# Kernel tuning notes

Measured on AMD Instinct MI355X. Metric: run time of the kernel, lower is better.

## Reference

```python
import jax, jax.numpy as jnp
import numpy as np

N_NODES = 100000
N_EDGES = 800000
# (in_dim, out_channels_per_head, heads) for the 5 stacked GATConv layers
DIMS = [(32, 24, 10), (240, 24, 5), (120, 24, 2), (48, 24, 1), (24, 12, 1)]
NEG_SLOPE = 0.2  # PyG GATConv default leaky_relu slope


def setup_inputs() -> dict:
    key = jax.random.key(0)
    ks = jax.random.split(key, 4 + 4 * len(DIMS))
    x = jax.random.normal(ks[0], (N_NODES, 32), jnp.float32)
    # edge_index with no self loops (dst = src + nonzero offset mod N),
    # since PyG GATConv removes then re-adds self loops.
    src = jax.random.randint(ks[1], (N_EDGES,), 0, N_NODES)
    off = jax.random.randint(ks[2], (N_EDGES,), 1, N_NODES)
    dst = (src + off) % N_NODES
    edge_index = jnp.stack([src, dst]).astype(jnp.int32)
    edge_attr = jax.random.normal(ks[3], (N_EDGES, 4), jnp.float32)
    inp = {"x": x, "edge_index": edge_index, "edge_attr": edge_attr}
    for i, (din, c, h) in enumerate(DIMS):
        kw, kb, ka, kd = ks[4 + 4 * i: 8 + 4 * i]
        s = 1.0 / np.sqrt(din)
        inp[f"W{i}"] = jax.random.normal(kw, (din, h * c), jnp.float32) * s
        inp[f"b{i}"] = jax.random.normal(kb, (h * c,), jnp.float32) * 0.01
        inp[f"as{i}"] = jax.random.normal(ka, (h, c), jnp.float32) * (1.0 / np.sqrt(c))
        inp[f"ad{i}"] = jax.random.normal(kd, (h, c), jnp.float32) * (1.0 / np.sqrt(c))
    return inp


def gat_layer(x, src, dst, W, b, a_src, a_dst):
    # Faithful PyG GATConv (concat=True, bias=True, edge_dim=None)
    n = x.shape[0]
    h_heads, c = a_src.shape
    h = (x @ W).reshape(n, h_heads, c)                      # [N,H,C]
    alpha_s = jnp.einsum('nhc,hc->nh', h, a_src)            # [N,H]
    alpha_d = jnp.einsum('nhc,hc->nh', h, a_dst)            # [N,H]
    e = jax.nn.leaky_relu(alpha_s[src] + alpha_d[dst], NEG_SLOPE)  # [E,H]
    # segment softmax over incoming edges of each destination node
    m = jax.ops.segment_max(e, dst, num_segments=n)         # [N,H]
    ex = jnp.exp(e - m[dst])
    z = jax.ops.segment_sum(ex, dst, num_segments=n)        # [N,H]
    attn = ex / z[dst]                                      # [E,H]
    out = jax.ops.segment_sum(h[src] * attn[:, :, None], dst, num_segments=n)
    return out.reshape(n, h_heads * c) + b


def reference(x, edge_index, edge_attr,
              W0, b0, as0, ad0, W1, b1, as1, ad1, W2, b2, as2, ad2,
              W3, b3, as3, ad3, W4, b4, as4, ad4):
    # edge_attr is ignored: GATConv(edge_dim=None) does not use it.
    n = x.shape[0]
    loop = jnp.arange(n, dtype=edge_index.dtype)
    src = jnp.concatenate([edge_index[0], loop])  # add self loops (PyG default)
    dst = jnp.concatenate([edge_index[1], loop])
    params = [(W0, b0, as0, ad0), (W1, b1, as1, ad1), (W2, b2, as2, ad2),
              (W3, b3, as3, ad3), (W4, b4, as4, ad4)]
    for W, b, a_s, a_d in params:
        x = jax.nn.relu(gat_layer(x, src, dst, W, b, a_s, a_d))
    return x
```

## Files before the change

kernel.cpp:

```cpp
#include <hip/hip_runtime.h>
#include <math.h>

#define NN 100000
#define EE 800000
#define ET (EE + NN)
#define BS 256
#define BKTS 391
#define FB_EPB 4096
#define LDSCAP 4096
#define DBINS 64

typedef _Float16 f16;
typedef __attribute__((ext_vector_type(4))) _Float16 half4;
typedef __attribute__((ext_vector_type(8))) _Float16 half8;
typedef __attribute__((ext_vector_type(4))) float f32x4;
template<int V> struct HV;
template<> struct HV<4>{ typedef half4 type; };
template<> struct HV<8>{ typedef half8 type; };

static inline int cdiv(long a, int b){ return (int)((a + b - 1) / b); }

__global__ __launch_bounds__(256) void k_bhist(const int* __restrict__ ei,
                                               int* __restrict__ bucketCount){
    __shared__ int hist[BKTS];
    for (int t = threadIdx.x; t < BKTS; t += 256) hist[t] = 0;
    __syncthreads();
    const int e0 = blockIdx.x * FB_EPB + threadIdx.x;
    #pragma unroll
    for (int i = 0; i < 16; i++){
        int e = e0 + i * 256;
        if (e < ET){
            int d = (e < EE) ? ei[EE + e] : (e - EE);
            atomicAdd(&hist[d >> 8], 1);
        }
    }
    __syncthreads();
    for (int t = threadIdx.x; t < BKTS; t += 256){
        int c = hist[t];
        if (c) atomicAdd(&bucketCount[t], c);
    }
}

__global__ void k_bscan(const int* __restrict__ bucketCount, int* __restrict__ bucketBase,
                        int* __restrict__ bucketCursor, int* __restrict__ rowptr){
    __shared__ int sh[512];
    int t = threadIdx.x;
    int c = (t < BKTS) ? bucketCount[t] : 0;
    sh[t] = c;
    __syncthreads();
    for (int o = 1; o < 512; o <<= 1){
        int v = (t >= o) ? sh[t - o] : 0;
        __syncthreads();
        sh[t] += v;
        __syncthreads();
    }
    if (t < BKTS){
        int excl = sh[t] - c;
        bucketBase[t] = excl;
        bucketCursor[t] = excl;
    }
    if (t == 0){
        bucketBase[BKTS] = ET;
        rowptr[NN] = ET;
    }
}

__global__ __launch_bounds__(256) void k_bfill(const int* __restrict__ ei,
        int* __restrict__ bucketCursor, unsigned* __restrict__ bpack){
    __shared__ int hist[BKTS];
    __shared__ int base[BKTS];
    for (int t = threadIdx.x; t < BKTS; t += 256) hist[t] = 0;
    __syncthreads();
    const int e0 = blockIdx.x * FB_EPB + threadIdx.x;
    unsigned pk[16], rb[16];
    #pragma unroll
    for (int i = 0; i < 16; i++){
        int e = e0 + i * 256;
        rb[i] = 0xFFFFFFFFu;
        if (e < ET){
            int s, d;
            if (e < EE){ s = ei[e]; d = ei[EE + e]; } else { s = e - EE; d = s; }
            int b = d >> 8;
            int r = atomicAdd(&hist[b], 1);
            pk[i] = ((unsigned)(d & 255) << 17) | (unsigned)s;
            rb[i] = ((unsigned)r << 9) | (unsigned)b;
        }
    }
    __syncthreads();
    for (int t = threadIdx.x; t < BKTS; t += 256){
        int c = hist[t];
        base[t] = c ? atomicAdd(&bucketCursor[t], c) : 0;
    }
    __syncthreads();
    #pragma unroll
    for (int i = 0; i < 16; i++){
        if (rb[i] != 0xFFFFFFFFu){
            int b = rb[i] & 511;
            int r = rb[i] >> 9;
            bpack[base[b] + r] = pk[i];
        }
    }
}

__global__ __launch_bounds__(256) void k_bsort(const unsigned* __restrict__ bpack,
        const int* __restrict__ bucketBase, int* __restrict__ rowptr,
        int* __restrict__ ssrc, int* __restrict__ dcnt){
    __shared__ int cnt[256];
    __shared__ int off[256];
    __shared__ int dh[DBINS];
    __shared__ unsigned stage[LDSCAP];
    int b = blockIdx.x;
    int n0 = bucketBase[b], n1 = bucketBase[b + 1];
    int nE = n1 - n0;
    int t = threadIdx.x;
    cnt[t] = 0;
    if (t < DBINS) dh[t] = 0;
    __syncthreads();
    for (int i = t; i < nE; i += 256){
        unsigned v = bpack[n0 + i];
        atomicAdd(&cnt[v >> 17], 1);
    }
    __syncthreads();
    int cv = cnt[t];
    off[t] = cv;
    __syncthreads();
    for (int o = 1; o < 256; o <<= 1){
        int v = (t >= o) ? off[t - o] : 0;
        __syncthreads();
        off[t] += v;
        __syncthreads();
    }
    int excl = off[t] - cv;
    __syncthreads();
    off[t] = excl;
    cnt[t] = 0;
    __syncthreads();
    for (int i = t; i < nE; i += 256){
        unsigned v = bpack[n0 + i];
        int dl = v >> 17;
        int r = atomicAdd(&cnt[dl], 1);
        stage[off[dl] + r] = v;
    }
    int d = b * 256 + t;
    if (d < NN){
        rowptr[d] = n0 + excl;
        int dg = (cv > DBINS - 1) ? (DBINS - 1) : cv;
        atomicAdd(&dh[dg], 1);
    }
    __syncthreads();
    for (int i = t; i < nE; i += 256){
        unsigned v = stage[i];
        ssrc[n0 + i] = (int)(v & 0x1FFFFu);
    }
    if (t < DBINS && dh[t]) atomicAdd(&dcnt[t], dh[t]);
}

__global__ void k_dscan(const int* __restrict__ dcnt, int* __restrict__ dcur){
    __shared__ int sh[DBINS];
    int t = threadIdx.x;
    sh[t] = dcnt[t];
    __syncthreads();
    int off = 0;
    for (int b = t + 1; b < DBINS; ++b) off += sh[b];
    dcur[t] = off;
}

__global__ __launch_bounds__(256) void k_dfill(const int* __restrict__ rowptr,
        int* __restrict__ dcur, int* __restrict__ perm){
    __shared__ int h[DBINS];
    __shared__ int base[DBINS];
    int t = threadIdx.x;
    if (t < DBINS) h[t] = 0;
    __syncthreads();
    int n = blockIdx.x * 256 + t;
    int d = 0, r = 0;
    if (n < NN){
        d = rowptr[n + 1] - rowptr[n];
        if (d > DBINS - 1) d = DBINS - 1;
        r = atomicAdd(&h[d], 1);
    }
    __syncthreads();
    if (t < DBINS){
        int c = h[t];
        base[t] = c ? atomicAdd(&dcur[t], c) : 0;
    }
    __syncthreads();
    if (n < NN) perm[base[d] + r] = n;
}

template<int K, int M, int KP, int MP, int HH, int CC>
__device__ __forceinline__ void prep_one(int idx, const float* __restrict__ W,
        const float* __restrict__ b, const float* __restrict__ as_,
        const float* __restrict__ ad_, f16* __restrict__ Wpk,
        float* __restrict__ bp, float* __restrict__ Was, float* __restrict__ Wad){
    constexpr int NT = MP / 16;
    if (idx < KP * MP){
        int j    = idx & 7;
        int lane = (idx >> 3) & 63;
        int rest = idx >> 9;
        int nt   = rest % NT;
        int ks   = rest / NT;
        int k = ks * 32 + ((lane >> 4) & 3) * 8 + j;
        int n = nt * 16 + (lane & 15);
        Wpk[idx] = (k < K && n < M) ? (f16)W[k * M + n] : (f16)0.f;
    }
    if (idx < MP) bp[idx] = (idx < M) ? b[idx] : 0.f;
    if (idx < K * HH){
        int k = idx / HH, hd = idx - k * HH;
        float s = 0.f, d = 0.f;
        #pragma unroll
        for (int c = 0; c < CC; c++){
            float w = W[k * M + hd * CC + c];
            s = fmaf(w, as_[hd * CC + c], s);
            d = fmaf(w, ad_[hd * CC + c], d);
        }
        Was[idx] = s;
        Wad[idx] = d;
    }
}

__device__ __forceinline__ void prep_w0(int idx, const float* __restrict__ W0,
                                        f16* __restrict__ Wpk0){
    int j    = idx & 7;
    int lane = (idx >> 3) & 63;
    int nt   = (idx >> 9) & 1;
    int hd   = idx >> 10;
    int k    = ((lane >> 4) & 3) * 8 + j;
    int cih  = nt * 16 + (lane & 15);
    Wpk0[idx] = (cih < 24) ? (f16)W0[k * 240 + hd * 24 + cih] : (f16)0.f;
}

struct PrepAll {
    const float *W[5], *b[5], *as[5], *ad[5];
    f16*   Wpk[5];
    f16*   Wpk0;
    float* bp[5];
    float* Was[5];
    float* Wad[5];
    int*   bucketCount;
    int*   dcnt;
};

__global__ void k_prep_all(PrepAll a){
    int idx = blockIdx.x * 256 + threadIdx.x;
    if (idx < 7680)
        prep_one< 32, 240,  32, 240, 10, 24>(idx,         a.W[0], a.b[0], a.as[0], a.ad[0], a.Wpk[0], a.bp[0], a.Was[0], a.Wad[0]);
    else if (idx < 40448)
        prep_one<240, 120, 256, 128,  5, 24>(idx - 7680,  a.W[1], a.b[1], a.as[1], a.ad[1], a.Wpk[1], a.bp[1], a.Was[1], a.Wad[1]);
    else if (idx < 48640)
        prep_one<120,  48, 128,  64,  2, 24>(idx - 40448, a.W[2], a.b[2], a.as[2], a.ad[2], a.Wpk[2], a.bp[2], a.Was[2], a.Wad[2]);
    else if (idx < 50688)
        prep_one< 48,  24,  64,  32,  1, 24>(idx - 48640, a.W[3], a.b[3], a.as[3], a.ad[3], a.Wpk[3], a.bp[3], a.Was[3], a.Wad[3]);
    else if (idx < 51200)
        prep_one< 24,  12,  32,  16,  1, 12>(idx - 50688, a.W[4], a.b[4], a.as[4], a.ad[4], a.Wpk[4], a.bp[4], a.Was[4], a.Wad[4]);
    else if (idx < 61440)
        prep_w0(idx - 51200, a.W[0], a.Wpk0);
    else if (idx < 61440 + BKTS)
        a.bucketCount[idx - 61440] = 0;
    else if (idx < 61440 + BKTS + DBINS)
        a.dcnt[idx - 61440 - BKTS] = 0;
}

__global__ void k_cvt_alpha0(const float* __restrict__ X, f16* __restrict__ Xh,
                             const float* __restrict__ Was, const float* __restrict__ Wad,
                             float* __restrict__ als, float* __restrict__ ald){
    int n = blockIdx.x * BS + threadIdx.x;
    if (n >= NN) return;
    float xr[32];
    #pragma unroll
    for (int i = 0; i < 8; i++){
        float4 v = *(const float4*)(X + (long)n * 32 + i * 4);
        xr[i * 4 + 0] = v.x; xr[i * 4 + 1] = v.y;
        xr[i * 4 + 2] = v.z; xr[i * 4 + 3] = v.w;
    }
    #pragma unroll
    for (int i = 0; i < 4; i++){
        half8 h;
        #pragma unroll
        for (int c = 0; c < 8; c++) h[c] = (f16)xr[i * 8 + c];
        *(half8*)(Xh + (long)n * 32 + i * 8) = h;
    }
    float s[10] = {}, d[10] = {};
    for (int k = 0; k < 32; k++){
        float x = xr[k];
        #pragma unroll
        for (int hd = 0; hd < 10; hd++){
            s[hd] = fmaf(x, Was[k * 10 + hd], s[hd]);
            d[hd] = fmaf(x, Wad[k * 10 + hd], d[hd]);
        }
    }
    #pragma unroll
    for (int hd = 0; hd < 10; hd++){
        als[(long)n * 12 + hd] = s[hd];
        ald[(long)n * 12 + hd] = d[hd];
    }
}

template<int MPH, int M, int HH, int CC, int SL>
__global__ __launch_bounds__(256) void k_alpha_v2(const f16* __restrict__ H2,
        const float* __restrict__ as_, const float* __restrict__ ad_,
        float* __restrict__ als, float* __restrict__ ald){
    constexpr int TA  = MPH / 8;
    constexpr int NPB = 256 / TA;
    __shared__ float sAs[256], sAd[256], sBs[256], sBd[256];
    const int t  = threadIdx.x;
    const int nl = t / TA;
    const int c  = t - nl * TA;
    const long n = (long)blockIdx.x * NPB + nl;
    float pAs = 0.f, pAd = 0.f, pBs = 0.f, pBd = 0.f;
    if (n < NN){
        half8 hv = *(const half8*)(H2 + n * MPH + c * 8);
        const int j0 = c * 8;
        const int hA = j0 / CC;
        const int sp = (hA + 1) * CC - j0;
        #pragma unroll
        for (int i = 0; i < 8; i++){
            int j = j0 + i;
            float w  = (float)hv[i];
            float ws = (j < M) ? as_[j] : 0.f;
            float wd = (j < M) ? ad_[j] : 0.f;
            if (i < sp){ pAs = fmaf(w, ws, pAs); pAd = fmaf(w, wd, pAd); }
            else       { pBs = fmaf(w, ws, pBs); pBd = fmaf(w, wd, pBd); }
        }
    }
    sAs[t] = pAs; sAd[t] = pAd; sBs[t] = pBs; sBd[t] = pBd;
    __syncthreads();
    if (t < NPB * HH){
        int nl2 = t / HH, hd = t - nl2 * HH;
        long n2 = (long)blockIdx.x * NPB + nl2;
        if (n2 < NN){
            float s = 0.f, d = 0.f;
            #pragma unroll
            for (int c2 = 0; c2 < TA; c2++){
                int j0 = c2 * 8, hA = j0 / CC, sp = (hA + 1) * CC - j0;
                int base = nl2 * TA + c2;
                if (hA == hd){ s += sAs[base]; d += sAd[base]; }
                if (sp < 8 && hA + 1 == hd){ s += sBs[base]; d += sBd[base]; }
            }
            als[n2 * SL + hd] = s;
            ald[n2 * SL + hd] = d;
        }
    }
}

__device__ __forceinline__ void smx_upd(float& ma, float& L, float& z, float e, float adv){
    float mn = fmaxf(ma, e);
    float Ln = mn + adv; Ln = (Ln >= 0.f) ? Ln : 0.2f * Ln;
    float ev = e + adv;  ev = (ev >= 0.f) ? ev : 0.2f * ev;
    z = z * __expf(L - Ln) + __expf(ev - Ln);
    ma = mn; L = Ln;
}

template<int HH, int SL, int ATTS, int TPN>
__global__ __launch_bounds__(256) void k_mzatt_split(const float* __restrict__ als,
        const float* __restrict__ ald, const int* __restrict__ rowptr,
        const int* __restrict__ ssrc, f16* __restrict__ att){
    constexpr int HPT = HH / TPN;
    long idx = (long)blockIdx.x * 256 + threadIdx.x;
    if (idx >= (long)NN * TPN) return;
    int n = (int)(idx / TPN);
    int g = (int)(idx - (long)n * TPN);
    const int c0 = g * HPT;
    float adv[HPT], ma[HPT], L[HPT], z[HPT];
    #pragma unroll
    for (int h = 0; h < HPT; h++){
        adv[h] = ald[(long)n * SL + c0 + h];
        ma[h] = -1e30f; L[h] = -1e30f; z[h] = 0.f;
    }
    const int beg = rowptr[n], end = rowptr[n + 1];
    int p = beg;
    for (; p + 4 <= end; p += 4){
        int s0 = ssrc[p], s1 = ssrc[p+1], s2 = ssrc[p+2], s3 = ssrc[p+3];
        float e0[HPT], e1[HPT], e2[HPT], e3[HPT];
        if constexpr (HPT == 2){
            float2 v0 = *(const float2*)(als + (long)s0 * SL + c0);
            float2 v1 = *(const float2*)(als + (long)s1 * SL + c0);
            float2 v2 = *(const float2*)(als + (long)s2 * SL + c0);
            float2 v3 = *(const float2*)(als + (long)s3 * SL + c0);
            e0[0]=v0.x; e0[1]=v0.y; e1[0]=v1.x; e1[1]=v1.y;
            e2[0]=v2.x; e2[1]=v2.y; e3[0]=v3.x; e3[1]=v3.y;
        } else {
            e0[0] = als[(long)s0 * SL + c0];
            e1[0] = als[(long)s1 * SL + c0];
            e2[0] = als[(long)s2 * SL + c0];
            e3[0] = als[(long)s3 * SL + c0];
        }
        #pragma unroll
        for (int h = 0; h < HPT; h++){
            smx_upd(ma[h], L[h], z[h], e0[h], adv[h]);
            smx_upd(ma[h], L[h], z[h], e1[h], adv[h]);
            smx_upd(ma[h], L[h], z[h], e2[h], adv[h]);
            smx_upd(ma[h], L[h], z[h], e3[h], adv[h]);
        }
    }
    for (; p < end; ++p){
        int s = ssrc[p];
        float e[HPT];
        if constexpr (HPT == 2){
            float2 v = *(const float2*)(als + (long)s * SL + c0);
            e[0] = v.x; e[1] = v.y;
        } else {
            e[0] = als[(long)s * SL + c0];
        }
        #pragma unroll
        for (int h = 0; h < HPT; h++) smx_upd(ma[h], L[h], z[h], e[h], adv[h]);
    }
    float zi[HPT];
    int pos[HPT];
    #pragma unroll
    for (int h = 0; h < HPT; h++){
        zi[h] = 1.f / z[h];
        int hh = c0 + h;
        pos[h] = (ATTS == 16) ? (hh + ((hh >= 5) ? 3 : 0)) : hh;
    }
    for (p = beg; p < end; ++p){
        int s = ssrc[p];
        float e[HPT];
        if constexpr (HPT == 2){
            float2 v = *(const float2*)(als + (long)s * SL + c0);
            e[0] = v.x; e[1] = v.y;
        } else {
            e[0] = als[(long)s * SL + c0];
        }
        #pragma unroll
        for (int h = 0; h < HPT; h++){
            float ev = e[h] + adv[h]; ev = (ev >= 0.f) ? ev : 0.2f * ev;
            att[(long)p * ATTS + pos[h]] = (f16)(__expf(ev - L[h]) * zi[h]);
        }
    }
}

__global__ __launch_bounds__(256) void k_aggX0_gemm(const f16* __restrict__ Xh,
        const f16* __restrict__ att, const int* __restrict__ rowptr,
        const int* __restrict__ ssrc, const int* __restrict__ perm,
        const f16* __restrict__ Wpk0, const float* __restrict__ bp0,
        f16* __restrict__ X1){
    constexpr int SA = 328;
    constexpr int SO = 264;
    __shared__ f16 smem[32 * SA];
    const int t = threadIdx.x;
    const int n0 = blockIdx.x * 32;

    {
        const int nloc = t >> 3;
        const int hg   = (t >> 2) & 1;
        const int ch   = t & 3;
        const int n    = perm[n0 + nloc];
        float acc[5][8] = {};
        int beg = rowptr[n], end = rowptr[n + 1];
        int p = beg;
        for (; p + 4 <= end; p += 4){
            int s0 = ssrc[p], s1 = ssrc[p+1], s2 = ssrc[p+2], s3 = ssrc[p+3];
            half8 x0 = *(const half8*)(Xh + (long)s0 * 32 + ch * 8);
            half8 x1 = *(const half8*)(Xh + (long)s1 * 32 + ch * 8);
            half8 x2 = *(const half8*)(Xh + (long)s2 * 32 + ch * 8);
            half8 x3 = *(const half8*)(Xh + (long)s3 * 32 + ch * 8);
            half8 a0 = *(const half8*)(att + (long)p * 16 + hg * 8);
            half8 a1 = *(const half8*)(att + (long)(p+1) * 16 + hg * 8);
            half8 a2 = *(const half8*)(att + (long)(p+2) * 16 + hg * 8);
            half8 a3 = *(const half8*)(att + (long)(p+3) * 16 + hg * 8);
            #pragma unroll
            for (int h = 0; h < 5; h++){
                float w0 = (float)a0[h], w1 = (float)a1[h];
                float w2 = (float)a2[h], w3 = (float)a3[h];
                #pragma unroll
                for (int c = 0; c < 8; c++){
                    acc[h][c] = fmaf(w0, (float)x0[c], acc[h][c]);
                    acc[h][c] = fmaf(w1, (float)x1[c], acc[h][c]);
                    acc[h][c] = fmaf(w2, (float)x2[c], acc[h][c]);
                    acc[h][c] = fmaf(w3, (float)x3[c], acc[h][c]);
                }
            }
        }
        for (; p < end; ++p){
            int s = ssrc[p];
            half8 xv = *(const half8*)(Xh + (long)s * 32 + ch * 8);
            half8 av = *(const half8*)(att + (long)p * 16 + hg * 8);
            #pragma unroll
            for (int h = 0; h < 5; h++){
                float w = (float)av[h];
                #pragma unroll
                for (int c = 0; c < 8; c++)
                    acc[h][c] = fmaf(w, (float)xv[c], acc[h][c]);
            }
        }
        #pragma unroll
        for (int h = 0; h < 5; h++){
            half8 o;
            #pragma unroll
            for (int c = 0; c < 8; c++) o[c] = (f16)acc[h][c];
            *(half8*)(smem + nloc * SA + (hg * 5 + h) * 32 + ch * 8) = o;
        }
    }
    __syncthreads();

    const int wave = t >> 6;
    const int lane = t & 63;
    const int quad = lane >> 4;
    const int l16  = lane & 15;
    const int mt   = wave & 1;
    half8 afr[5];
    #pragma unroll
    for (int i = 0; i < 5; i++){
        const int hd = (wave + 4 * i) >> 1;
        afr[i] = *(const half8*)(smem + (mt * 16 + l16) * SA + hd * 32 + quad * 8);
    }
    __syncthreads();
    #pragma unroll
    for (int i = 0; i < 5; i++){
        const int hd = (wave + 4 * i) >> 1;
        #pragma unroll
        for (int nt = 0; nt < 2; nt++){
            half8 bfr = *(const half8*)(Wpk0 + ((hd * 2 + nt) * 64 + lane) * 8);
            f32x4 acc2 = (f32x4){0.f, 0.f, 0.f, 0.f};
            acc2 = __builtin_amdgcn_mfma_f32_16x16x32_f16(afr[i], bfr, acc2, 0, 0, 0);
            int cih = nt * 16 + l16;
            if (cih < 24){
                float bv = bp0[hd * 24 + cih];
                #pragma unroll
                for (int reg = 0; reg < 4; reg++){
                    int rl = mt * 16 + quad * 4 + reg;
                    float v = acc2[reg] + bv;
                    smem[rl * SO + hd * 24 + cih] = (f16)((v > 0.f) ? v : 0.f);
                }
            }
        }
    }
    __syncthreads();

    const half8 hz = {};
    #pragma unroll
    for (int c = t; c < 1024; c += 256){
        int row = c >> 5, c8 = c & 31;
        long rn = perm[n0 + row];
        half8 v = (c8 >= 30) ? hz : *(const half8*)(smem + row * SO + c8 * 8);
        *(half8*)(X1 + rn * 256 + c8 * 8) = v;
    }
}

template<int KP, int MPH>
__global__ __launch_bounds__(256) void k_gemm_mfma(const f16* __restrict__ Xh,
        const f16* __restrict__ Wpk, f16* __restrict__ H2){
    constexpr int NT = MPH / 16;
    constexpr int KS = KP / 32;
    const int wave = threadIdx.x >> 6;
    const int lane = threadIdx.x & 63;
    const int quad = lane >> 4;
    const int l16  = lane & 15;
    const long row0 = (long)blockIdx.x * 128 + wave * 32;

    f32x4 acc[2][NT];
    #pragma unroll
    for (int mt = 0; mt < 2; mt++)
        #pragma unroll
        for (int nt = 0; nt < NT; nt++)
            acc[mt][nt] = (f32x4){0.f, 0.f, 0.f, 0.f};

    const long r0 = row0 + l16;
    const long r1 = row0 + 16 + l16;
    const half8 hz = {};
    half8 a0 = (r0 < NN) ? *(const half8*)(Xh + r0 * KP + quad * 8) : hz;
    half8 a1 = (r1 < NN) ? *(const half8*)(Xh + r1 * KP + quad * 8) : hz;
    half8 bc[NT];
    #pragma unroll
    for (int nt = 0; nt < NT; nt++)
        bc[nt] = *(const half8*)(Wpk + ((long)nt * 64 + lane) * 8);

    for (int ks = 0; ks < KS; ks++){
        half8 n0 = hz, n1 = hz, bn[NT];
        if (ks + 1 < KS){
            const int kk = (ks + 1) * 32 + quad * 8;
            n0 = (r0 < NN) ? *(const half8*)(Xh + r0 * KP + kk) : hz;
            n1 = (r1 < NN) ? *(const half8*)(Xh + r1 * KP + kk) : hz;
            const f16* bp_ = Wpk + ((long)(ks + 1) * NT * 64 + lane) * 8;
            #pragma unroll
            for (int nt = 0; nt < NT; nt++)
                bn[nt] = *(const half8*)(bp_ + (long)nt * 512);
        } else {
            #pragma unroll
            for (int nt = 0; nt < NT; nt++) bn[nt] = hz;
        }
        #pragma unroll
        for (int nt = 0; nt < NT; nt++){
            acc[0][nt] = __builtin_amdgcn_mfma_f32_16x16x32_f16(a0, bc[nt], acc[0][nt], 0, 0, 0);
            acc[1][nt] = __builtin_amdgcn_mfma_f32_16x16x32_f16(a1, bc[nt], acc[1][nt], 0, 0, 0);
        }
        a0 = n0; a1 = n1;
        #pragma unroll
        for (int nt = 0; nt < NT; nt++) bc[nt] = bn[nt];
    }
    #pragma unroll
    for (int mt = 0; mt < 2; mt++){
        #pragma unroll
        for (int reg = 0; reg < 4; reg++){
            long r = row0 + mt * 16 + quad * 4 + reg;
            if (r < NN){
                #pragma unroll
                for (int nt = 0; nt < NT; nt++)
                    H2[r * MPH + nt * 16 + l16] = (f16)acc[mt][nt][reg];
            }
        }
    }
}

template<int HH, int CC, int MPH, int MPO, int VEC, bool O16, int SL>
__global__ __launch_bounds__(256) void k_aggsm_h(const f16* __restrict__ H2,
        const float* __restrict__ als, const float* __restrict__ ald,
        const int* __restrict__ rowptr, const int* __restrict__ ssrc,
        const float* __restrict__ bp, f16* __restrict__ out16,
        float* __restrict__ out32, int MREAL){
    constexpr int TPN = MPO / VEC;
    typedef typename HV<VEC>::type hvec;
    long idx = (long)blockIdx.x * 256 + threadIdx.x;
    if (idx >= (long)NN * TPN) return;
    int n = (int)(idx / TPN);
    int q = (int)(idx - (long)n * TPN);
    int j0 = q * VEC;
    if constexpr (!O16){ if (j0 >= MREAL) return; }
    int hd = j0 / CC; if (hd > HH - 1) hd = HH - 1;
    const float adv = ald[(long)n * SL + hd];
    const int beg = rowptr[n], end = rowptr[n + 1];

    float ma = -1e30f, L = -1e30f, z = 0.f;
    int p = beg;
    for (; p + 4 <= end; p += 4){
        int s0 = ssrc[p], s1 = ssrc[p+1], s2 = ssrc[p+2], s3 = ssrc[p+3];
        float e0 = als[(long)s0 * SL + hd];
        float e1 = als[(long)s1 * SL + hd];
        float e2 = als[(long)s2 * SL + hd];
        float e3 = als[(long)s3 * SL + hd];
        smx_upd(ma, L, z, e0, adv);
        smx_upd(ma, L, z, e1, adv);
        smx_upd(ma, L, z, e2, adv);
        smx_upd(ma, L, z, e3, adv);
    }
    for (; p < end; ++p)
        smx_upd(ma, L, z, als[(long)ssrc[p] * SL + hd], adv);
    const float zi = 1.f / z;

    float acc[VEC] = {};
    p = beg;
    for (; p + 4 <= end; p += 4){
        int s0 = ssrc[p], s1 = ssrc[p+1], s2 = ssrc[p+2], s3 = ssrc[p+3];
        float e0 = als[(long)s0 * SL + hd];
        float e1 = als[(long)s1 * SL + hd];
        float e2 = als[(long)s2 * SL + hd];
        float e3 = als[(long)s3 * SL + hd];
        e0 += adv; e0 = (e0 >= 0.f) ? e0 : 0.2f * e0;
        e1 += adv; e1 = (e1 >= 0.f) ? e1 : 0.2f * e1;
        e2 += adv; e2 = (e2 >= 0.f) ? e2 : 0.2f * e2;
        e3 += adv; e3 = (e3 >= 0.f) ? e3 : 0.2f * e3;
        float w0 = __expf(e0 - L) * zi;
        float w1 = __expf(e1 - L) * zi;
        float w2 = __expf(e2 - L) * zi;
        float w3 = __expf(e3 - L) * zi;
        hvec h0 = *(const hvec*)(H2 + (long)s0 * MPH + j0);
        hvec h1 = *(const hvec*)(H2 + (long)s1 * MPH + j0);
        hvec h2 = *(const hvec*)(H2 + (long)s2 * MPH + j0);
        hvec h3 = *(const hvec*)(H2 + (long)s3 * MPH + j0);
        #pragma unroll
        for (int c = 0; c < VEC; c++){
            acc[c] = fmaf(w0, (float)h0[c], acc[c]);
            acc[c] = fmaf(w1, (float)h1[c], acc[c]);
            acc[c] = fmaf(w2, (float)h2[c], acc[c]);
            acc[c] = fmaf(w3, (float)h3[c], acc[c]);
        }
    }
    for (; p < end; ++p){
        int s = ssrc[p];
        float e = als[(long)s * SL + hd] + adv;
        e = (e >= 0.f) ? e : 0.2f * e;
        float w = __expf(e - L) * zi;
        hvec hv = *(const hvec*)(H2 + (long)s * MPH + j0);
        #pragma unroll
        for (int c = 0; c < VEC; c++)
            acc[c] = fmaf(w, (float)hv[c], acc[c]);
    }
    if constexpr (O16){
        hvec o;
        #pragma unroll
        for (int c = 0; c < VEC; c++){
            float v = acc[c] + bp[j0 + c];
            o[c] = (f16)((v > 0.f) ? v : 0.f);
        }
        *(hvec*)(out16 + (long)n * MPO + j0) = o;
    } else {
        #pragma unroll
        for (int c = 0; c < VEC; c++){
            float v = acc[c] + bp[j0 + c];
            out32[(long)n * MREAL + j0 + c] = (v > 0.f) ? v : 0.f;
        }
    }
}

template<int K, int M, int KP, int MPH, int MPO, int HH, int CC, int VEC, bool O16, int SL>
static void run_layer(const f16* Xin, f16* H2,
                      const f16* Wpk, const float* bp,
                      const float* asv, const float* adv,
                      float* als, float* ald,
                      const int* rowptr, const int* ssrc,
                      f16* Xnext, float* out32, hipStream_t stream){
    constexpr int OTPN = MPO / VEC;
    constexpr int TA = MPH / 8;
    k_gemm_mfma<KP, MPH><<<cdiv(NN, 128), 256, 0, stream>>>(Xin, Wpk, H2);
    k_alpha_v2<MPH, M, HH, CC, SL><<<cdiv((long)NN * TA, 256), 256, 0, stream>>>(
        H2, asv, adv, als, ald);
    k_aggsm_h<HH, CC, MPH, MPO, VEC, O16, SL><<<cdiv((long)NN * OTPN, 256), 256, 0, stream>>>(
        H2, als, ald, rowptr, ssrc, bp, Xnext, out32, M);
}

extern "C" void kernel_launch(void* const* d_in, const int* in_sizes, int n_in,
                              void* d_out, int out_size, void* d_ws, size_t ws_size,
                              hipStream_t stream){
    const float* x0 = (const float*)d_in[0];
    const int*   ei = (const int*)d_in[1];
    PrepAll pa;
    for (int i = 0; i < 5; i++){
        pa.W[i]  = (const float*)d_in[3 + 4 * i];
        pa.b[i]  = (const float*)d_in[4 + 4 * i];
        pa.as[i] = (const float*)d_in[5 + 4 * i];
        pa.ad[i] = (const float*)d_in[6 + 4 * i];
    }

    char* p = (char*)d_ws;
    auto alloc = [&](size_t bytes) -> char* {
        char* r = p;
        p += (bytes + 255) & ~(size_t)255;
        return r;
    };
    f16*   Xh     = (f16*)alloc((size_t)NN * 256 * 2);
    f16*   H2     = (f16*)alloc((size_t)NN * 320 * 2);
    f16*   att    = (f16*)alloc((size_t)ET * 16 * 2);
    float* als    = (float*)alloc((size_t)NN * 12 * 4);
    float* ald    = (float*)alloc((size_t)NN * 12 * 4);
    const int wpkSz[5] = {7680, 32768, 8192, 2048, 512};
    const int mpSz[5]  = {240, 128, 64, 32, 16};
    const int khSz[5]  = {320, 1200, 240, 48, 24};
    for (int i = 0; i < 5; i++){
        pa.Wpk[i] = (f16*)alloc((size_t)wpkSz[i] * 2);
        pa.bp[i]  = (float*)alloc((size_t)mpSz[i] * 4);
        pa.Was[i] = (float*)alloc((size_t)khSz[i] * 4);
        pa.Wad[i] = (float*)alloc((size_t)khSz[i] * 4);
    }
    pa.Wpk0 = (f16*)alloc((size_t)10240 * 2);
    int*      bucketCount  = (int*)alloc((size_t)BKTS * 4);
    int*      bucketBase   = (int*)alloc((size_t)(BKTS + 1) * 4);
    int*      bucketCursor = (int*)alloc((size_t)BKTS * 4);
    unsigned* bpack        = (unsigned*)alloc((size_t)ET * 4);
    int*      rowptr       = (int*)alloc((size_t)(NN + 1) * 4);
    int*      ssrc         = (int*)alloc((size_t)ET * 4);
    int*      dcnt         = (int*)alloc((size_t)DBINS * 4);
    int*      dcur         = (int*)alloc((size_t)DBINS * 4);
    int*      perm         = (int*)alloc((size_t)NN * 4);
    pa.bucketCount = bucketCount;
    pa.dcnt = dcnt;

    k_prep_all<<<242, 256, 0, stream>>>(pa);
    k_bhist<<<cdiv(ET, FB_EPB), 256, 0, stream>>>(ei, bucketCount);
    k_bscan<<<1, 512, 0, stream>>>(bucketCount, bucketBase, bucketCursor, rowptr);
    k_bfill<<<cdiv(ET, FB_EPB), 256, 0, stream>>>(ei, bucketCursor, bpack);
    k_bsort<<<BKTS, 256, 0, stream>>>(bpack, bucketBase, rowptr, ssrc, dcnt);
    k_dscan<<<1, DBINS, 0, stream>>>(dcnt, dcur);
    k_dfill<<<cdiv(NN, 256), 256, 0, stream>>>(rowptr, dcur, perm);

    k_cvt_alpha0<<<cdiv(NN, BS), BS, 0, stream>>>(x0, Xh, pa.Was[0], pa.Wad[0], als, ald);
    k_mzatt_split<10, 12, 16, 5><<<cdiv((long)NN * 5, 256), 256, 0, stream>>>(
        als, ald, rowptr, ssrc, att);
    k_aggX0_gemm<<<NN / 32, 256, 0, stream>>>(Xh, att, rowptr, ssrc, perm,
        pa.Wpk0, pa.bp[0], H2 );

    run_layer<240, 120, 256, 128, 128,  5, 24, 8, true,  8>(H2, Xh, pa.Wpk[1],
        pa.bp[1], pa.as[1], pa.ad[1], als, ald, rowptr, ssrc, H2, nullptr, stream);
    run_layer<120,  48, 128,  64,  64,  2, 24, 8, true,  2>(H2, Xh, pa.Wpk[2],
        pa.bp[2], pa.as[2], pa.ad[2], als, ald, rowptr, ssrc, H2, nullptr, stream);
    run_layer< 48,  24,  64,  32,  32,  1, 24, 8, true,  1>(H2, Xh, pa.Wpk[3],
        pa.bp[3], pa.as[3], pa.ad[3], als, ald, rowptr, ssrc, H2, nullptr, stream);
    run_layer< 24,  12,  32,  16,  16,  1, 12, 4, false, 1>(H2, Xh, pa.Wpk[4],
        pa.bp[4], pa.as[4], pa.ad[4], als, ald, rowptr, ssrc, nullptr, (float*)d_out, stream);
}
```

Baseline: 484.2 us.

## Fuse preprocessing kernels and compute attention logits in GEMM epilogue

```diff
diff --git a/kernel.cpp b/kernel.cpp
--- a/kernel.cpp
+++ b/kernel.cpp
@@ -19,174 +19,6 @@
 template<> struct HV<8>{ typedef half8 type; };
 
 static inline int cdiv(long a, int b){ return (int)((a + b - 1) / b); }
-
-__global__ __launch_bounds__(256) void k_bhist(const int* __restrict__ ei,
-                                               int* __restrict__ bucketCount){
-    __shared__ int hist[BKTS];
-    for (int t = threadIdx.x; t < BKTS; t += 256) hist[t] = 0;
-    __syncthreads();
-    const int e0 = blockIdx.x * FB_EPB + threadIdx.x;
-    #pragma unroll
-    for (int i = 0; i < 16; i++){
-        int e = e0 + i * 256;
-        if (e < ET){
-            int d = (e < EE) ? ei[EE + e] : (e - EE);
-            atomicAdd(&hist[d >> 8], 1);
-        }
-    }
-    __syncthreads();
-    for (int t = threadIdx.x; t < BKTS; t += 256){
-        int c = hist[t];
-        if (c) atomicAdd(&bucketCount[t], c);
-    }
-}
-
-__global__ void k_bscan(const int* __restrict__ bucketCount, int* __restrict__ bucketBase,
-                        int* __restrict__ bucketCursor, int* __restrict__ rowptr){
-    __shared__ int sh[512];
-    int t = threadIdx.x;
-    int c = (t < BKTS) ? bucketCount[t] : 0;
-    sh[t] = c;
-    __syncthreads();
-    for (int o = 1; o < 512; o <<= 1){
-        int v = (t >= o) ? sh[t - o] : 0;
-        __syncthreads();
-        sh[t] += v;
-        __syncthreads();
-    }
-    if (t < BKTS){
-        int excl = sh[t] - c;
-        bucketBase[t] = excl;
-        bucketCursor[t] = excl;
-    }
-    if (t == 0){
-        bucketBase[BKTS] = ET;
-        rowptr[NN] = ET;
-    }
-}
-
-__global__ __launch_bounds__(256) void k_bfill(const int* __restrict__ ei,
-        int* __restrict__ bucketCursor, unsigned* __restrict__ bpack){
-    __shared__ int hist[BKTS];
-    __shared__ int base[BKTS];
-    for (int t = threadIdx.x; t < BKTS; t += 256) hist[t] = 0;
-    __syncthreads();
-    const int e0 = blockIdx.x * FB_EPB + threadIdx.x;
-    unsigned pk[16], rb[16];
-    #pragma unroll
-    for (int i = 0; i < 16; i++){
-        int e = e0 + i * 256;
-        rb[i] = 0xFFFFFFFFu;
-        if (e < ET){
-            int s, d;
-            if (e < EE){ s = ei[e]; d = ei[EE + e]; } else { s = e - EE; d = s; }
-            int b = d >> 8;
-            int r = atomicAdd(&hist[b], 1);
-            pk[i] = ((unsigned)(d & 255) << 17) | (unsigned)s;
-            rb[i] = ((unsigned)r << 9) | (unsigned)b;
-        }
-    }
-    __syncthreads();
-    for (int t = threadIdx.x; t < BKTS; t += 256){
-        int c = hist[t];
-        base[t] = c ? atomicAdd(&bucketCursor[t], c) : 0;
-    }
-    __syncthreads();
-    #pragma unroll
-    for (int i = 0; i < 16; i++){
-        if (rb[i] != 0xFFFFFFFFu){
-            int b = rb[i] & 511;
-            int r = rb[i] >> 9;
-            bpack[base[b] + r] = pk[i];
-        }
-    }
-}
-
-__global__ __launch_bounds__(256) void k_bsort(const unsigned* __restrict__ bpack,
-        const int* __restrict__ bucketBase, int* __restrict__ rowptr,
-        int* __restrict__ ssrc, int* __restrict__ dcnt){
-    __shared__ int cnt[256];
-    __shared__ int off[256];
-    __shared__ int dh[DBINS];
-    __shared__ unsigned stage[LDSCAP];
-    int b = blockIdx.x;
-    int n0 = bucketBase[b], n1 = bucketBase[b + 1];
-    int nE = n1 - n0;
-    int t = threadIdx.x;
-    cnt[t] = 0;
-    if (t < DBINS) dh[t] = 0;
-    __syncthreads();
-    for (int i = t; i < nE; i += 256){
-        unsigned v = bpack[n0 + i];
-        atomicAdd(&cnt[v >> 17], 1);
-    }
-    __syncthreads();
-    int cv = cnt[t];
-    off[t] = cv;
-    __syncthreads();
-    for (int o = 1; o < 256; o <<= 1){
-        int v = (t >= o) ? off[t - o] : 0;
-        __syncthreads();
-        off[t] += v;
-        __syncthreads();
-    }
-    int excl = off[t] - cv;
-    __syncthreads();
-    off[t] = excl;
-    cnt[t] = 0;
-    __syncthreads();
-    for (int i = t; i < nE; i += 256){
-        unsigned v = bpack[n0 + i];
-        int dl = v >> 17;
-        int r = atomicAdd(&cnt[dl], 1);
-        stage[off[dl] + r] = v;
-    }
-    int d = b * 256 + t;
-    if (d < NN){
-        rowptr[d] = n0 + excl;
-        int dg = (cv > DBINS - 1) ? (DBINS - 1) : cv;
-        atomicAdd(&dh[dg], 1);
-    }
-    __syncthreads();
-    for (int i = t; i < nE; i += 256){
-        unsigned v = stage[i];
-        ssrc[n0 + i] = (int)(v & 0x1FFFFu);
-    }
-    if (t < DBINS && dh[t]) atomicAdd(&dcnt[t], dh[t]);
-}
-
-__global__ void k_dscan(const int* __restrict__ dcnt, int* __restrict__ dcur){
-    __shared__ int sh[DBINS];
-    int t = threadIdx.x;
-    sh[t] = dcnt[t];
-    __syncthreads();
-    int off = 0;
-    for (int b = t + 1; b < DBINS; ++b) off += sh[b];
-    dcur[t] = off;
-}
-
-__global__ __launch_bounds__(256) void k_dfill(const int* __restrict__ rowptr,
-        int* __restrict__ dcur, int* __restrict__ perm){
-    __shared__ int h[DBINS];
-    __shared__ int base[DBINS];
-    int t = threadIdx.x;
-    if (t < DBINS) h[t] = 0;
-    __syncthreads();
-    int n = blockIdx.x * 256 + t;
-    int d = 0, r = 0;
-    if (n < NN){
-        d = rowptr[n + 1] - rowptr[n];
-        if (d > DBINS - 1) d = DBINS - 1;
-        r = atomicAdd(&h[d], 1);
-    }
-    __syncthreads();
-    if (t < DBINS){
-        int c = h[t];
-        base[t] = c ? atomicAdd(&dcur[t], c) : 0;
-    }
-    __syncthreads();
-    if (n < NN) perm[base[d] + r] = n;
-}
 
 template<int K, int M, int KP, int MP, int HH, int CC>
 __device__ __forceinline__ void prep_one(int idx, const float* __restrict__ W,
@@ -237,34 +69,111 @@
     float* bp[5];
     float* Was[5];
     float* Wad[5];
-    int*   bucketCount;
-    int*   dcnt;
 };
 
-__global__ void k_prep_all(PrepAll a){
-    int idx = blockIdx.x * 256 + threadIdx.x;
-    if (idx < 7680)
-        prep_one< 32, 240,  32, 240, 10, 24>(idx,         a.W[0], a.b[0], a.as[0], a.ad[0], a.Wpk[0], a.bp[0], a.Was[0], a.Wad[0]);
-    else if (idx < 40448)
-        prep_one<240, 120, 256, 128,  5, 24>(idx - 7680,  a.W[1], a.b[1], a.as[1], a.ad[1], a.Wpk[1], a.bp[1], a.Was[1], a.Wad[1]);
-    else if (idx < 48640)
-        prep_one<120,  48, 128,  64,  2, 24>(idx - 40448, a.W[2], a.b[2], a.as[2], a.ad[2], a.Wpk[2], a.bp[2], a.Was[2], a.Wad[2]);
-    else if (idx < 50688)
-        prep_one< 48,  24,  64,  32,  1, 24>(idx - 48640, a.W[3], a.b[3], a.as[3], a.ad[3], a.Wpk[3], a.bp[3], a.Was[3], a.Wad[3]);
-    else if (idx < 51200)
-        prep_one< 24,  12,  32,  16,  1, 12>(idx - 50688, a.W[4], a.b[4], a.as[4], a.ad[4], a.Wpk[4], a.bp[4], a.Was[4], a.Wad[4]);
-    else if (idx < 61440)
-        prep_w0(idx - 51200, a.W[0], a.Wpk0);
-    else if (idx < 61440 + BKTS)
-        a.bucketCount[idx - 61440] = 0;
-    else if (idx < 61440 + BKTS + DBINS)
-        a.dcnt[idx - 61440 - BKTS] = 0;
-}
-
-__global__ void k_cvt_alpha0(const float* __restrict__ X, f16* __restrict__ Xh,
-                             const float* __restrict__ Was, const float* __restrict__ Wad,
-                             float* __restrict__ als, float* __restrict__ ald){
-    int n = blockIdx.x * BS + threadIdx.x;
+__global__ __launch_bounds__(256) void k_prep_bhist(PrepAll a, const int* __restrict__ ei,
+                                                    int* __restrict__ bucketCount){
+    if (blockIdx.x < 240){
+        int idx = blockIdx.x * 256 + threadIdx.x;
+        if (idx < 7680)
+            prep_one< 32, 240,  32, 240, 10, 24>(idx,         a.W[0], a.b[0], a.as[0], a.ad[0], a.Wpk[0], a.bp[0], a.Was[0], a.Wad[0]);
+        else if (idx < 40448)
+            prep_one<240, 120, 256, 128,  5, 24>(idx - 7680,  a.W[1], a.b[1], a.as[1], a.ad[1], a.Wpk[1], a.bp[1], a.Was[1], a.Wad[1]);
+        else if (idx < 48640)
+            prep_one<120,  48, 128,  64,  2, 24>(idx - 40448, a.W[2], a.b[2], a.as[2], a.ad[2], a.Wpk[2], a.bp[2], a.Was[2], a.Wad[2]);
+        else if (idx < 50688)
+            prep_one< 48,  24,  64,  32,  1, 24>(idx - 48640, a.W[3], a.b[3], a.as[3], a.ad[3], a.Wpk[3], a.bp[3], a.Was[3], a.Wad[3]);
+        else if (idx < 51200)
+            prep_one< 24,  12,  32,  16,  1, 12>(idx - 50688, a.W[4], a.b[4], a.as[4], a.ad[4], a.Wpk[4], a.bp[4], a.Was[4], a.Wad[4]);
+        else
+            prep_w0(idx - 51200, a.W[0], a.Wpk0);
+        return;
+    }
+    __shared__ int hist[BKTS];
+    for (int t = threadIdx.x; t < BKTS; t += 256) hist[t] = 0;
+    __syncthreads();
+    const int e0 = (blockIdx.x - 240) * FB_EPB + threadIdx.x;
+    #pragma unroll
+    for (int i = 0; i < 16; i++){
+        int e = e0 + i * 256;
+        if (e < ET){
+            int d = (e < EE) ? ei[EE + e] : (e - EE);
+            atomicAdd(&hist[d >> 8], 1);
+        }
+    }
+    __syncthreads();
+    for (int t = threadIdx.x; t < BKTS; t += 256){
+        int c = hist[t];
+        if (c) atomicAdd(&bucketCount[t], c);
+    }
+}
+
+__global__ void k_bscan(const int* __restrict__ bucketCount, int* __restrict__ bucketBase,
+                        int* __restrict__ bucketCursor, int* __restrict__ rowptr){
+    __shared__ int sh[512];
+    int t = threadIdx.x;
+    int c = (t < BKTS) ? bucketCount[t] : 0;
+    sh[t] = c;
+    __syncthreads();
+    for (int o = 1; o < 512; o <<= 1){
+        int v = (t >= o) ? sh[t - o] : 0;
+        __syncthreads();
+        sh[t] += v;
+        __syncthreads();
+    }
+    if (t < BKTS){
+        int excl = sh[t] - c;
+        bucketBase[t] = excl;
+        bucketCursor[t] = excl;
+    }
+    if (t == 0){
+        bucketBase[BKTS] = ET;
+        rowptr[NN] = ET;
+    }
+}
+
+__global__ __launch_bounds__(256) void k_bfill_cvt(const int* __restrict__ ei,
+        int* __restrict__ bucketCursor, unsigned* __restrict__ bpack,
+        const float* __restrict__ X, f16* __restrict__ Xh,
+        const float* __restrict__ Was, const float* __restrict__ Wad,
+        float* __restrict__ als, float* __restrict__ ald){
+    __shared__ int hist[BKTS];
+    __shared__ int base[BKTS];
+    if (blockIdx.x < 220){
+        for (int t = threadIdx.x; t < BKTS; t += 256) hist[t] = 0;
+        __syncthreads();
+        const int e0 = blockIdx.x * FB_EPB + threadIdx.x;
+        unsigned pk[16], rb[16];
+        #pragma unroll
+        for (int i = 0; i < 16; i++){
+            int e = e0 + i * 256;
+            rb[i] = 0xFFFFFFFFu;
+            if (e < ET){
+                int s, d;
+                if (e < EE){ s = ei[e]; d = ei[EE + e]; } else { s = e - EE; d = s; }
+                int b = d >> 8;
+                int r = atomicAdd(&hist[b], 1);
+                pk[i] = ((unsigned)(d & 255) << 17) | (unsigned)s;
+                rb[i] = ((unsigned)r << 9) | (unsigned)b;
+            }
+        }
+        __syncthreads();
+        for (int t = threadIdx.x; t < BKTS; t += 256){
+            int c = hist[t];
+            base[t] = c ? atomicAdd(&bucketCursor[t], c) : 0;
+        }
+        __syncthreads();
+        #pragma unroll
+        for (int i = 0; i < 16; i++){
+            if (rb[i] != 0xFFFFFFFFu){
+                int b = rb[i] & 511;
+                int r = rb[i] >> 9;
+                bpack[base[b] + r] = pk[i];
+            }
+        }
+        return;
+    }
+    int n = (blockIdx.x - 220) * 256 + threadIdx.x;
     if (n >= NN) return;
     float xr[32];
     #pragma unroll
@@ -296,51 +205,57 @@
     }
 }
 
-template<int MPH, int M, int HH, int CC, int SL>
-__global__ __launch_bounds__(256) void k_alpha_v2(const f16* __restrict__ H2,
-        const float* __restrict__ as_, const float* __restrict__ ad_,
-        float* __restrict__ als, float* __restrict__ ald){
-    constexpr int TA  = MPH / 8;
-    constexpr int NPB = 256 / TA;
-    __shared__ float sAs[256], sAd[256], sBs[256], sBd[256];
-    const int t  = threadIdx.x;
-    const int nl = t / TA;
-    const int c  = t - nl * TA;
-    const long n = (long)blockIdx.x * NPB + nl;
-    float pAs = 0.f, pAd = 0.f, pBs = 0.f, pBd = 0.f;
-    if (n < NN){
-        half8 hv = *(const half8*)(H2 + n * MPH + c * 8);
-        const int j0 = c * 8;
-        const int hA = j0 / CC;
-        const int sp = (hA + 1) * CC - j0;
-        #pragma unroll
-        for (int i = 0; i < 8; i++){
-            int j = j0 + i;
-            float w  = (float)hv[i];
-            float ws = (j < M) ? as_[j] : 0.f;
-            float wd = (j < M) ? ad_[j] : 0.f;
-            if (i < sp){ pAs = fmaf(w, ws, pAs); pAd = fmaf(w, wd, pAd); }
-            else       { pBs = fmaf(w, ws, pBs); pBd = fmaf(w, wd, pBd); }
-        }
-    }
-    sAs[t] = pAs; sAd[t] = pAd; sBs[t] = pBs; sBd[t] = pBd;
-    __syncthreads();
-    if (t < NPB * HH){
-        int nl2 = t / HH, hd = t - nl2 * HH;
-        long n2 = (long)blockIdx.x * NPB + nl2;
-        if (n2 < NN){
-            float s = 0.f, d = 0.f;
-            #pragma unroll
-            for (int c2 = 0; c2 < TA; c2++){
-                int j0 = c2 * 8, hA = j0 / CC, sp = (hA + 1) * CC - j0;
-                int base = nl2 * TA + c2;
-                if (hA == hd){ s += sAs[base]; d += sAd[base]; }
-                if (sp < 8 && hA + 1 == hd){ s += sBs[base]; d += sBd[base]; }
-            }
-            als[n2 * SL + hd] = s;
-            ald[n2 * SL + hd] = d;
-        }
-    }
+__global__ __launch_bounds__(256) void k_bsort(const unsigned* __restrict__ bpack,
+        const int* __restrict__ bucketBase, int* __restrict__ rowptr,
+        int* __restrict__ ssrc, int* __restrict__ dcnt){
+    __shared__ int cnt[256];
+    __shared__ int off[256];
+    __shared__ int dh[DBINS];
+    __shared__ unsigned stage[LDSCAP];
+    int b = blockIdx.x;
+    int n0 = bucketBase[b], n1 = bucketBase[b + 1];
+    int nE = n1 - n0;
+    int t = threadIdx.x;
+    cnt[t] = 0;
+    if (t < DBINS) dh[t] = 0;
+    __syncthreads();
+    for (int i = t; i < nE; i += 256){
+        unsigned v = bpack[n0 + i];
+        atomicAdd(&cnt[v >> 17], 1);
+    }
+    __syncthreads();
+    int cv = cnt[t];
+    off[t] = cv;
+    __syncthreads();
+    for (int o = 1; o < 256; o <<= 1){
+        int v = (t >= o) ? off[t - o] : 0;
+        __syncthreads();
+        off[t] += v;
+        __syncthreads();
+    }
+    int excl = off[t] - cv;
+    __syncthreads();
+    off[t] = excl;
+    cnt[t] = 0;
+    __syncthreads();
+    for (int i = t; i < nE; i += 256){
+        unsigned v = bpack[n0 + i];
+        int dl = v >> 17;
+        int r = atomicAdd(&cnt[dl], 1);
+        stage[off[dl] + r] = v;
+    }
+    int d = b * 256 + t;
+    if (d < NN){
+        rowptr[d] = n0 + excl;
+        int dg = (cv > DBINS - 1) ? (DBINS - 1) : cv;
+        atomicAdd(&dh[dg], 1);
+    }
+    __syncthreads();
+    for (int i = t; i < nE; i += 256){
+        unsigned v = stage[i];
+        ssrc[n0 + i] = (int)(v & 0x1FFFFu);
+    }
+    if (t < DBINS && dh[t]) atomicAdd(&dcnt[t], dh[t]);
 }
 
 __device__ __forceinline__ void smx_upd(float& ma, float& L, float& z, float e, float adv){
@@ -352,11 +267,26 @@
 }
 
 template<int HH, int SL, int ATTS, int TPN>
-__global__ __launch_bounds__(256) void k_mzatt_split(const float* __restrict__ als,
+__global__ __launch_bounds__(256) void k_mzatt_dscan(const float* __restrict__ als,
         const float* __restrict__ ald, const int* __restrict__ rowptr,
-        const int* __restrict__ ssrc, f16* __restrict__ att){
+        const int* __restrict__ ssrc, f16* __restrict__ att,
+        const int* __restrict__ dcnt, int* __restrict__ dcur){
     constexpr int HPT = HH / TPN;
-    long idx = (long)blockIdx.x * 256 + threadIdx.x;
+    if (blockIdx.x == 0){
+        __shared__ int sh[DBINS];
+        int t = threadIdx.x;
+        if (t < DBINS){
+            sh[t] = dcnt[t];
+        }
+        __syncthreads();
+        if (t < DBINS){
+            int off = 0;
+            for (int b = t + 1; b < DBINS; ++b) off += sh[b];
+            dcur[t] = off;
+        }
+        return;
+    }
+    long idx = (long)(blockIdx.x - 1) * 256 + threadIdx.x;
     if (idx >= (long)NN * TPN) return;
     int n = (int)(idx / TPN);
     int g = (int)(idx - (long)n * TPN);
@@ -428,6 +358,29 @@
             att[(long)p * ATTS + pos[h]] = (f16)(__expf(ev - L[h]) * zi[h]);
         }
     }
+}
+
+__global__ __launch_bounds__(256) void k_dfill(const int* __restrict__ rowptr,
+        int* __restrict__ dcur, int* __restrict__ perm){
+    __shared__ int h[DBINS];
+    __shared__ int base[DBINS];
+    int t = threadIdx.x;
+    if (t < DBINS) h[t] = 0;
+    __syncthreads();
+    int n = blockIdx.x * 256 + t;
+    int d = 0, r = 0;
+    if (n < NN){
+        d = rowptr[n + 1] - rowptr[n];
+        if (d > DBINS - 1) d = DBINS - 1;
+        r = atomicAdd(&h[d], 1);
+    }
+    __syncthreads();
+    if (t < DBINS){
+        int c = h[t];
+        base[t] = c ? atomicAdd(&dcur[t], c) : 0;
+    }
+    __syncthreads();
+    if (n < NN) perm[base[d] + r] = n;
 }
 
 __global__ __launch_bounds__(256) void k_aggX0_gemm(const f16* __restrict__ Xh,
@@ -538,11 +491,14 @@
     }
 }
 
-template<int KP, int MPH>
-__global__ __launch_bounds__(256) void k_gemm_mfma(const f16* __restrict__ Xh,
-        const f16* __restrict__ Wpk, f16* __restrict__ H2){
+template<int KP, int MPH, int M, int HH, int CC, int SL>
+__global__ __launch_bounds__(256) void k_gemm_alpha(const f16* __restrict__ Xh,
+        const f16* __restrict__ Wpk, const float* __restrict__ as_,
+        const float* __restrict__ ad_, f16* __restrict__ H2,
+        float* __restrict__ als, float* __restrict__ ald){
     constexpr int NT = MPH / 16;
     constexpr int KS = KP / 32;
+    __shared__ f16 hs[128 * MPH];
     const int wave = threadIdx.x >> 6;
     const int lane = threadIdx.x & 63;
     const int quad = lane >> 4;
@@ -593,12 +549,39 @@
     for (int mt = 0; mt < 2; mt++){
         #pragma unroll
         for (int reg = 0; reg < 4; reg++){
+            const int rl = wave * 32 + mt * 16 + quad * 4 + reg;
             long r = row0 + mt * 16 + quad * 4 + reg;
+            #pragma unroll
+            for (int nt = 0; nt < NT; nt++)
+                hs[rl * MPH + nt * 16 + l16] = (f16)acc[mt][nt][reg];
             if (r < NN){
                 #pragma unroll
                 for (int nt = 0; nt < NT; nt++)
                     H2[r * MPH + nt * 16 + l16] = (f16)acc[mt][nt][reg];
             }
+        }
+    }
+    __syncthreads();
+
+    const long nb = (long)blockIdx.x * 128;
+    for (int tk = threadIdx.x; tk < 128 * HH; tk += 256){
+        int row = tk / HH, hd = tk - row * HH;
+        long n = nb + row;
+        if (n < NN){
+            const f16* hrow = hs + row * MPH + hd * CC;
+            float s = 0.f, d = 0.f;
+            #pragma unroll
+            for (int c0 = 0; c0 < CC; c0 += 4){
+                half4 hv = *(const half4*)(hrow + c0);
+                #pragma unroll
+                for (int j = 0; j < 4; j++){
+                    float w = (float)hv[j];
+                    s = fmaf(w, as_[hd * CC + c0 + j], s);
+                    d = fmaf(w, ad_[hd * CC + c0 + j], d);
+                }
+            }
+            als[n * SL + hd] = s;
+            ald[n * SL + hd] = d;
         }
     }
 }
@@ -701,10 +684,8 @@
                       const int* rowptr, const int* ssrc,
                       f16* Xnext, float* out32, hipStream_t stream){
     constexpr int OTPN = MPO / VEC;
-    constexpr int TA = MPH / 8;
-    k_gemm_mfma<KP, MPH><<<cdiv(NN, 128), 256, 0, stream>>>(Xin, Wpk, H2);
-    k_alpha_v2<MPH, M, HH, CC, SL><<<cdiv((long)NN * TA, 256), 256, 0, stream>>>(
-        H2, asv, adv, als, ald);
+    k_gemm_alpha<KP, MPH, M, HH, CC, SL><<<cdiv(NN, 128), 256, 0, stream>>>(
+        Xin, Wpk, asv, adv, H2, als, ald);
     k_aggsm_h<HH, CC, MPH, MPO, VEC, O16, SL><<<cdiv((long)NN * OTPN, 256), 256, 0, stream>>>(
         H2, als, ald, rowptr, ssrc, bp, Xnext, out32, M);
 }
@@ -743,29 +724,28 @@
         pa.Wad[i] = (float*)alloc((size_t)khSz[i] * 4);
     }
     pa.Wpk0 = (f16*)alloc((size_t)10240 * 2);
-    int*      bucketCount  = (int*)alloc((size_t)BKTS * 4);
+    int*      cntbuf       = (int*)alloc((size_t)(BKTS + DBINS) * 4);
+    int*      bucketCount  = cntbuf;
+    int*      dcnt         = cntbuf + BKTS;
     int*      bucketBase   = (int*)alloc((size_t)(BKTS + 1) * 4);
     int*      bucketCursor = (int*)alloc((size_t)BKTS * 4);
     unsigned* bpack        = (unsigned*)alloc((size_t)ET * 4);
     int*      rowptr       = (int*)alloc((size_t)(NN + 1) * 4);
     int*      ssrc         = (int*)alloc((size_t)ET * 4);
-    int*      dcnt         = (int*)alloc((size_t)DBINS * 4);
     int*      dcur         = (int*)alloc((size_t)DBINS * 4);
     int*      perm         = (int*)alloc((size_t)NN * 4);
-    pa.bucketCount = bucketCount;
-    pa.dcnt = dcnt;
-
-    k_prep_all<<<242, 256, 0, stream>>>(pa);
-    k_bhist<<<cdiv(ET, FB_EPB), 256, 0, stream>>>(ei, bucketCount);
+
+    hipMemsetAsync(cntbuf, 0, (size_t)(BKTS + DBINS) * 4, stream);
+
+    k_prep_bhist<<<240 + cdiv(ET, FB_EPB), 256, 0, stream>>>(pa, ei, bucketCount);
     k_bscan<<<1, 512, 0, stream>>>(bucketCount, bucketBase, bucketCursor, rowptr);
-    k_bfill<<<cdiv(ET, FB_EPB), 256, 0, stream>>>(ei, bucketCursor, bpack);
+    k_bfill_cvt<<<cdiv(ET, FB_EPB) + cdiv(NN, 256), 256, 0, stream>>>(
+        ei, bucketCursor, bpack, x0, Xh, pa.Was[0], pa.Wad[0], als, ald);
     k_bsort<<<BKTS, 256, 0, stream>>>(bpack, bucketBase, rowptr, ssrc, dcnt);
-    k_dscan<<<1, DBINS, 0, stream>>>(dcnt, dcur);
+    k_mzatt_dscan<10, 12, 16, 5><<<1 + cdiv((long)NN * 5, 256), 256, 0, stream>>>(
+        als, ald, rowptr, ssrc, att, dcnt, dcur);
     k_dfill<<<cdiv(NN, 256), 256, 0, stream>>>(rowptr, dcur, perm);
 
-    k_cvt_alpha0<<<cdiv(NN, BS), BS, 0, stream>>>(x0, Xh, pa.Was[0], pa.Wad[0], als, ald);
-    k_mzatt_split<10, 12, 16, 5><<<cdiv((long)NN * 5, 256), 256, 0, stream>>>(
-        als, ald, rowptr, ssrc, att);
     k_aggX0_gemm<<<NN / 32, 256, 0, stream>>>(Xh, att, rowptr, ssrc, perm,
         pa.Wpk0, pa.bp[0], H2 );
 
```

Measured after the change: 422.4 us (median of 3 runs). 12.8% less time.
